# Kernel tuning notes

Hardware: AMD Instinct MI355X
Metric: run time of the kernel (lower is better)

The kernel has to match this reference:

```python
import jax, jax.numpy as jnp
import numpy as np

H = 1024  # hidden_size
V = 32000  # vocab_size
L = 2048  # y_len


def _lstm_cell(gates, c):
    # torch gate order: input, forget, cell(g), output
    i = jax.nn.sigmoid(gates[:H])
    f = jax.nn.sigmoid(gates[H:2 * H])
    g = jnp.tanh(gates[2 * H:3 * H])
    o = jax.nn.sigmoid(gates[3 * H:4 * H])
    c_new = f * c + i * g
    return o * jnp.tanh(c_new), c_new


def setup_inputs() -> dict:
    key = jax.random.key(0)
    ks = jax.random.split(key, 13)
    s = 0.05
    inp = {
        "y": jax.random.randint(ks[0], (L,), 0, V, dtype=jnp.int32),
        "context_vector": jax.random.normal(ks[1], (2, H), dtype=jnp.float32),
        # layer 0: input dim 1
        "w_ih0": jax.random.normal(ks[2], (4 * H, 1), dtype=jnp.float32) * s,
        "w_hh0": jax.random.normal(ks[3], (4 * H, H), dtype=jnp.float32) * s,
        "b_ih0": jax.random.normal(ks[4], (4 * H,), dtype=jnp.float32) * s,
        "b_hh0": jax.random.normal(ks[5], (4 * H,), dtype=jnp.float32) * s,
        # layer 1: input dim H
        "w_ih1": jax.random.normal(ks[6], (4 * H, H), dtype=jnp.float32) * s,
        "w_hh1": jax.random.normal(ks[7], (4 * H, H), dtype=jnp.float32) * s,
        "b_ih1": jax.random.normal(ks[8], (4 * H,), dtype=jnp.float32) * s,
        "b_hh1": jax.random.normal(ks[9], (4 * H,), dtype=jnp.float32) * s,
        # fc: hidden -> vocab
        "w_fc": jax.random.normal(ks[10], (V, H), dtype=jnp.float32) * s,
        "b_fc": jax.random.normal(ks[11], (V,), dtype=jnp.float32) * s,
    }
    return inp


def reference(y, context_vector, w_ih0, w_hh0, b_ih0, b_hh0,
              w_ih1, w_hh1, b_ih1, b_hh1, w_fc, b_fc):
    # tfr = 0.0 => teacher forcing never used; next input is argmax of predictions.
    # h_s = h_c = context_vector initially (as in the torch module).
    def step(carry, _):
        tok, h, c = carry  # tok: scalar f32; h,c: [2, H]
        x = tok[None]  # [1]
        g0 = w_ih0 @ x + b_ih0 + w_hh0 @ h[0] + b_hh0
        h0, c0 = _lstm_cell(g0, c[0])
        g1 = w_ih1 @ h0 + b_ih1 + w_hh1 @ h[1] + b_hh1
        h1, c1 = _lstm_cell(g1, c[1])
        preds = jax.nn.relu(w_fc @ h1 + b_fc)  # [V]
        best = jnp.argmax(preds).astype(jnp.float32)
        return (best, jnp.stack([h0, h1]), jnp.stack([c0, c1])), preds

    init = (y[0].astype(jnp.float32), context_vector, context_vector)
    _, preds_seq = jax.lax.scan(step, init, None, length=L - 1)  # [L-1, V]
    outputs = jnp.concatenate(
        [jnp.zeros((1, V), dtype=jnp.float32), preds_seq], axis=0)  # [L, V]
    return outputs  # training mode: raw outputs (eval would apply log_softmax)
```

## Files before the change

kernel.cpp:

```cpp
#include <hip/hip_runtime.h>
#include <cstdint>
#include <cstddef>

#define H   1024
#define V   32000
#define L   2048
#define G4  4096
#define NB  256
#define NT  1024
#define RPB (V / NB)

#define GNB   500
#define GT    512
#define GS    8
#define GR    8
#define NCHUNK (L / GS)

__device__ __forceinline__ float wave_reduce_sum(float v) {
    #pragma unroll
    for (int off = 32; off > 0; off >>= 1) v += __shfl_down(v, off);
    return v;
}

__device__ __forceinline__ float wave_reduce_max(float v) {
    #pragma unroll
    for (int off = 32; off > 0; off >>= 1) v = fmaxf(v, __shfl_down(v, off));
    return v;
}

__device__ __forceinline__ unsigned long long wave_reduce_max_u64(unsigned long long v) {
    #pragma unroll
    for (int off = 32; off > 0; off >>= 1) {
        const unsigned long long o = __shfl_down(v, off);
        v = (o > v) ? o : v;
    }
    return v;
}

__device__ __forceinline__ float sigmoidf_(float x) {
    return 1.0f / (1.0f + expf(-x));
}

__device__ __forceinline__ float dot4(const float4 w, const float* __restrict__ h, int c) {
    return w.x * h[c] + w.y * h[c + 1] + w.z * h[c + 2] + w.w * h[c + 3];
}

__device__ __forceinline__ float sb2f(int w, int pos) {
    return (float)((w << ((3 - pos) * 8)) >> 24);
}

__global__ __launch_bounds__(256) void quant_fc(
    const float* __restrict__ src, signed char* __restrict__ dst,
    float2* __restrict__ scl_eps, unsigned int* __restrict__ emax_bits)
{
    const int gw   = (blockIdx.x * blockDim.x + threadIdx.x) >> 6;
    const int lane = threadIdx.x & 63;
    const int nw   = (gridDim.x * blockDim.x) >> 6;
    for (int row = gw; row < V; row += nw) {
        const float* p = src + (size_t)row * H + lane * 16;
        float w[16];
        #pragma unroll
        for (int j = 0; j < 4; j++) {
            const float4 f = *(const float4*)(p + j * 4);
            w[j * 4 + 0] = f.x; w[j * 4 + 1] = f.y;
            w[j * 4 + 2] = f.z; w[j * 4 + 3] = f.w;
        }
        float m = 0.f;
        #pragma unroll
        for (int j = 0; j < 16; j++) m = fmaxf(m, fabsf(w[j]));
        m = wave_reduce_max(m);
        m = __shfl(m, 0);
        const float scale = fmaxf(m, 1e-30f) / 127.f;
        const float inv   = 127.f / fmaxf(m, 1e-30f);
        int q[16];
        float esq = 0.f;
        #pragma unroll
        for (int j = 0; j < 16; j++) {
            q[j] = __float2int_rn(w[j] * inv);
            const float e = w[j] - scale * (float)q[j];
            esq += e * e;
        }
        esq = wave_reduce_sum(esq);
        const unsigned int d0 = (q[0] & 255) | ((q[1] & 255) << 8) | ((q[2] & 255) << 16) | ((unsigned int)(q[3] & 255) << 24);
        const unsigned int d1 = (q[4] & 255) | ((q[5] & 255) << 8) | ((q[6] & 255) << 16) | ((unsigned int)(q[7] & 255) << 24);
        const unsigned int d2 = (q[8] & 255) | ((q[9] & 255) << 8) | ((q[10] & 255) << 16) | ((unsigned int)(q[11] & 255) << 24);
        const unsigned int d3 = (q[12] & 255) | ((q[13] & 255) << 8) | ((q[14] & 255) << 16) | ((unsigned int)(q[15] & 255) << 24);
        *(int4*)(dst + (size_t)row * H + lane * 16) =
            make_int4((int)d0, (int)d1, (int)d2, (int)d3);
        if (lane == 0) {
            const float e2 = sqrtf(esq) + 1e-12f;
            scl_eps[row] = make_float2(scale, e2);
            atomicMax(emax_bits, __float_as_uint(e2));
        }
    }
}

__global__ __launch_bounds__(NT) void init_kernel(
    const int* __restrict__ y, const float* __restrict__ ctx,
    const float* __restrict__ w_hh0, const float* __restrict__ b_ih0,
    const float* __restrict__ b_hh0,
    const float* __restrict__ w_hh1, const float* __restrict__ b_ih1,
    const float* __restrict__ b_hh1,
    float* __restrict__ v0, float* __restrict__ u1,
    float* __restrict__ c0, float* __restrict__ c1,
    float* __restrict__ h1g, unsigned long long* __restrict__ keys)
{
    __shared__ __align__(16) float h0s[H];
    __shared__ __align__(16) float h1s[H];
    const int b = blockIdx.x, t = threadIdx.x;
    h0s[t] = ctx[t];
    h1s[t] = ctx[H + t];
    __syncthreads();

    const int wave = t >> 6, lane = t & 63;
    const int rowR = (wave >> 2) * H + b * 4 + (wave & 3);
    {
        const float* w0r = w_hh0 + (size_t)rowR * H;
        const float* w1r = w_hh1 + (size_t)rowR * H;
        float accV = 0.f, accU = 0.f;
        #pragma unroll
        for (int k = 0; k < 4; k++) {
            const int c = k * 256 + lane * 4;
            accV += dot4(*(const float4*)(w0r + c), h0s, c);
            accU += dot4(*(const float4*)(w1r + c), h1s, c);
        }
        accV = wave_reduce_sum(accV);
        accU = wave_reduce_sum(accU);
        if (lane == 0) {
            v0[rowR] = accV + b_ih0[rowR] + b_hh0[rowR];
            u1[rowR] = accU + b_ih1[rowR] + b_hh1[rowR];
        }
    }
    if (b == 0) {
        c0[t]  = ctx[t];
        c1[t]  = ctx[H + t];
        h1g[t] = ctx[H + t];
        if (t < NB) keys[t] = 0ull;
        if (t == 0) {
            keys[0] = ((unsigned long long)0x7F800000u << 32) |
                      (0xFFFFFFFFu - (unsigned int)y[0]);
        }
    }
}

__global__ __launch_bounds__(NT) void lstm_kernel(
    const float* __restrict__ w_ih0, const float* __restrict__ w_ih1,
    const float* __restrict__ w_hh0,
    const float* __restrict__ b_ih0, const float* __restrict__ b_hh0,
    const float* __restrict__ v0_in, float* __restrict__ v0_out,
    const float* __restrict__ u1,
    const float* __restrict__ c0_in, float* __restrict__ c0_out,
    float* __restrict__ c1, float* __restrict__ h1g,
    const unsigned long long* __restrict__ keys,
    float* __restrict__ h1_hist, const int step)
{
    __shared__ __align__(16) float h0s[H];
    __shared__ float g1s[16];
    __shared__ unsigned long long kred[4];
    const int b = blockIdx.x, t = threadIdx.x;
    const int wave = t >> 6, lane = t & 63;

    if (wave < 4) {
        unsigned long long k = keys[t];
        k = wave_reduce_max_u64(k);
        if (lane == 0) kred[wave] = k;
    }
    __syncthreads();
    unsigned long long kk = kred[0];
    kk = (kred[1] > kk) ? kred[1] : kk;
    kk = (kred[2] > kk) ? kred[2] : kk;
    kk = (kred[3] > kk) ? kred[3] : kk;
    const float tok =
        (float)(unsigned int)(0xFFFFFFFFu - (unsigned int)(kk & 0xFFFFFFFFull));

    {
        const float gi = v0_in[t]         + tok * w_ih0[t];
        const float gf = v0_in[H + t]     + tok * w_ih0[H + t];
        const float gg = v0_in[2 * H + t] + tok * w_ih0[2 * H + t];
        const float go = v0_in[3 * H + t] + tok * w_ih0[3 * H + t];
        const float i_ = sigmoidf_(gi);
        const float f_ = sigmoidf_(gf);
        const float g_ = tanhf(gg);
        const float o_ = sigmoidf_(go);
        const float cn = f_ * c0_in[t] + i_ * g_;
        if (b == 0) c0_out[t] = cn;
        h0s[t] = o_ * tanhf(cn);
    }
    __syncthreads();

    const int rowR = (wave >> 2) * H + b * 4 + (wave & 3);
    {
        const float* wA = w_ih1 + (size_t)rowR * H;
        const float* wB = w_hh0 + (size_t)rowR * H;
        float accA = 0.f, accB = 0.f;
        #pragma unroll
        for (int k = 0; k < 4; k++) {
            const int c = k * 256 + lane * 4;
            accA += dot4(*(const float4*)(wA + c), h0s, c);
            accB += dot4(*(const float4*)(wB + c), h0s, c);
        }
        accA = wave_reduce_sum(accA);
        accB = wave_reduce_sum(accB);
        if (lane == 0) {
            g1s[wave]    = accA + u1[rowR];
            v0_out[rowR] = accB + b_ih0[rowR] + b_hh0[rowR];
        }
    }
    __syncthreads();

    if (t < 4) {
        const float i_ = sigmoidf_(g1s[t]);
        const float f_ = sigmoidf_(g1s[4 + t]);
        const float g_ = tanhf(g1s[8 + t]);
        const float o_ = sigmoidf_(g1s[12 + t]);
        const float cn = f_ * c1[b * 4 + t] + i_ * g_;
        c1[b * 4 + t] = cn;
        const float hv = o_ * tanhf(cn);
        h1g[b * 4 + t] = hv;
        if (h1_hist) h1_hist[(size_t)step * H + b * 4 + t] = hv;
    }
}

__global__ __launch_bounds__(NT) void screen_kernel(
    const signed char* __restrict__ wq8, const float2* __restrict__ scl_eps,
    const unsigned int* __restrict__ emax_bits,
    const float* __restrict__ w_fc, const float* __restrict__ b_fc,
    const float* __restrict__ w_hh1, const float* __restrict__ b_ih1,
    const float* __restrict__ b_hh1,
    const float* __restrict__ h1g, float* __restrict__ u1,
    unsigned long long* __restrict__ keys)
{
    __shared__ __align__(16) float h1s[H];
    __shared__ float aprx[128];
    __shared__ float red[16];
    __shared__ float Amax_s, Hl2_s;
    __shared__ unsigned long long wkey[16];
    const int b = blockIdx.x, t = threadIdx.x;
    const int wave = t >> 6, lane = t & 63;

    h1s[t] = h1g[t];
    if (t < 128) aprx[t] = -1.f;
    __syncthreads();

    {
        float sq = h1s[t] * h1s[t];
        sq = wave_reduce_sum(sq);
        if (lane == 0) red[wave] = sq;
    }

    const float4 hA = *(const float4*)(h1s + lane * 16);
    const float4 hB = *(const float4*)(h1s + lane * 16 + 4);
    const float4 hC = *(const float4*)(h1s + lane * 16 + 8);
    const float4 hD = *(const float4*)(h1s + lane * 16 + 12);

    #pragma unroll
    for (int i = 0; i < 8; i++) {
        const int rl = i * 16 + wave;
        if (rl >= RPB) break;
        const int row = b * RPB + rl;
        const int4 qv = *(const int4*)(wq8 + (size_t)row * H + lane * 16);
        float acc;
        acc  = sb2f(qv.x, 0) * hA.x + sb2f(qv.x, 1) * hA.y + sb2f(qv.x, 2) * hA.z + sb2f(qv.x, 3) * hA.w;
        acc += sb2f(qv.y, 0) * hB.x + sb2f(qv.y, 1) * hB.y + sb2f(qv.y, 2) * hB.z + sb2f(qv.y, 3) * hB.w;
        acc += sb2f(qv.z, 0) * hC.x + sb2f(qv.z, 1) * hC.y + sb2f(qv.z, 2) * hC.z + sb2f(qv.z, 3) * hC.w;
        acc += sb2f(qv.w, 0) * hD.x + sb2f(qv.w, 1) * hD.y + sb2f(qv.w, 2) * hD.z + sb2f(qv.w, 3) * hD.w;
        acc = wave_reduce_sum(acc);
        if (lane == 0) {
            float p = scl_eps[row].x * acc + b_fc[row];
            p = p > 0.f ? p : 0.f;
            aprx[rl] = p;
        }
    }
    __syncthreads();

    if (t == 0) {
        float s = 0.f;
        #pragma unroll
        for (int i = 0; i < 16; i++) s += red[i];
        Hl2_s = sqrtf(s);
    }
    if (wave == 0) {
        float m = fmaxf(aprx[lane], aprx[lane + 64]);
        m = wave_reduce_max(m);
        if (lane == 0) Amax_s = m;
    }
    __syncthreads();

    const float emax   = __uint_as_float(*emax_bits);
    const float thresh = Amax_s - (2.f * emax * Hl2_s + 1e-3f);

    unsigned long long bestKey = 0ull;

    #pragma unroll
    for (int i = 0; i < 8; i++) {
        const int rl = i * 16 + wave;
        if (rl >= RPB) break;
        const float av = aprx[rl];
        if (av >= thresh) {
            const int row = b * RPB + rl;
            const float* wrow = w_fc + (size_t)row * H;
            float acc = 0.f;
            #pragma unroll
            for (int k = 0; k < 4; k++) {
                const int c = k * 256 + lane * 4;
                acc += dot4(*(const float4*)(wrow + c), h1s, c);
            }
            acc = wave_reduce_sum(acc);
            if (lane == 0) {
                float p = acc + b_fc[row];
                p = p > 0.f ? p : 0.f;
                const unsigned long long key =
                    ((unsigned long long)__float_as_uint(p) << 32) |
                    (0xFFFFFFFFu - (unsigned int)row);
                if (key > bestKey) bestKey = key;
            }
        }
    }

    {
        const int rowR = (wave >> 2) * H + b * 4 + (wave & 3);
        const float* wrow = w_hh1 + (size_t)rowR * H;
        float acc = 0.f;
        #pragma unroll
        for (int k = 0; k < 4; k++) {
            const int c = k * 256 + lane * 4;
            acc += dot4(*(const float4*)(wrow + c), h1s, c);
        }
        acc = wave_reduce_sum(acc);
        if (lane == 0) u1[rowR] = acc + b_ih1[rowR] + b_hh1[rowR];
    }

    if (lane == 0) wkey[wave] = bestKey;
    __syncthreads();
    if (t == 0) {
        unsigned long long k = wkey[0];
        #pragma unroll
        for (int i = 1; i < 16; i++) k = (wkey[i] > k) ? wkey[i] : k;
        keys[b] = k;
    }
}

__global__ __launch_bounds__(NT) void fc32_kernel(
    const float* __restrict__ w_fc, const float* __restrict__ b_fc,
    const float* __restrict__ w_hh1, const float* __restrict__ b_ih1,
    const float* __restrict__ b_hh1,
    const float* __restrict__ h1g, float* __restrict__ u1,
    unsigned long long* __restrict__ keys, float* __restrict__ out_row)
{
    __shared__ __align__(16) float h1s[H];
    __shared__ unsigned long long wkey[16];
    const int b = blockIdx.x, t = threadIdx.x;
    const int wave = t >> 6, lane = t & 63;

    h1s[t] = h1g[t];
    __syncthreads();

    unsigned long long bestKey = 0ull;
    #pragma unroll
    for (int i = 0; i < 8; i++) {
        const int rl = i * 16 + wave;
        if (rl >= RPB) break;
        const int row = b * RPB + rl;
        const float* wrow = w_fc + (size_t)row * H;
        float acc = 0.f;
        #pragma unroll
        for (int k = 0; k < 4; k++) {
            const int c = k * 256 + lane * 4;
            acc += dot4(*(const float4*)(wrow + c), h1s, c);
        }
        acc = wave_reduce_sum(acc);
        if (lane == 0) {
            float p = acc + b_fc[row];
            p = p > 0.f ? p : 0.f;
            out_row[row] = p;
            const unsigned long long key =
                ((unsigned long long)__float_as_uint(p) << 32) |
                (0xFFFFFFFFu - (unsigned int)row);
            if (key > bestKey) bestKey = key;
        }
    }

    {
        const int rowR = (wave >> 2) * H + b * 4 + (wave & 3);
        const float* wrow = w_hh1 + (size_t)rowR * H;
        float acc = 0.f;
        #pragma unroll
        for (int k = 0; k < 4; k++) {
            const int c = k * 256 + lane * 4;
            acc += dot4(*(const float4*)(wrow + c), h1s, c);
        }
        acc = wave_reduce_sum(acc);
        if (lane == 0) u1[rowR] = acc + b_ih1[rowR] + b_hh1[rowR];
    }

    if (lane == 0) wkey[wave] = bestKey;
    __syncthreads();
    if (t == 0) {
        unsigned long long k = wkey[0];
        #pragma unroll
        for (int i = 1; i < 16; i++) k = (wkey[i] > k) ? wkey[i] : k;
        keys[b] = k;
    }
}

__global__ __launch_bounds__(GT) void out_gemm(
    const float* __restrict__ w_fc, const float* __restrict__ b_fc,
    const float* __restrict__ h1_hist, float* __restrict__ out)
{
    __shared__ __align__(16) float hs[GS][H];
    __shared__ float stage[GS][64];
    const int b = blockIdx.x, t = threadIdx.x;
    const int wave = t >> 6, lane = t & 63;
    const int row0 = b * 64 + wave * GR;

    float4 wr[GR][4];
    #pragma unroll
    for (int r = 0; r < GR; r++)
        #pragma unroll
        for (int k = 0; k < 4; k++)
            wr[r][k] = *(const float4*)(w_fc + (size_t)(row0 + r) * H + k * 256 + lane * 4);

    for (int chunk = 0; chunk < NCHUNK; ++chunk) {
        __syncthreads();
        {
            const float4* src = (const float4*)(h1_hist + (size_t)chunk * GS * H);
            float4* dsts = (float4*)(&hs[0][0]);
            #pragma unroll
            for (int j = 0; j < 4; j++) dsts[j * GT + t] = src[j * GT + t];
        }
        __syncthreads();

        #pragma unroll
        for (int sb = 0; sb < 2; sb++) {
            float acc[GR][4];
            #pragma unroll
            for (int r = 0; r < GR; r++)
                #pragma unroll
                for (int s = 0; s < 4; s++) acc[r][s] = 0.f;
            #pragma unroll
            for (int k = 0; k < 4; k++) {
                const int c = k * 256 + lane * 4;
                const float4 h0 = *(const float4*)(&hs[sb * 4 + 0][c]);
                const float4 h1 = *(const float4*)(&hs[sb * 4 + 1][c]);
                const float4 h2 = *(const float4*)(&hs[sb * 4 + 2][c]);
                const float4 h3 = *(const float4*)(&hs[sb * 4 + 3][c]);
                #pragma unroll
                for (int r = 0; r < GR; r++) {
                    const float4 w = wr[r][k];
                    acc[r][0] += w.x * h0.x + w.y * h0.y + w.z * h0.z + w.w * h0.w;
                    acc[r][1] += w.x * h1.x + w.y * h1.y + w.z * h1.z + w.w * h1.w;
                    acc[r][2] += w.x * h2.x + w.y * h2.y + w.z * h2.z + w.w * h2.w;
                    acc[r][3] += w.x * h3.x + w.y * h3.y + w.z * h3.z + w.w * h3.w;
                }
            }
            #pragma unroll
            for (int r = 0; r < GR; r++)
                #pragma unroll
                for (int s = 0; s < 4; s++) {
                    const float vv = wave_reduce_sum(acc[r][s]);
                    if (lane == 0) stage[sb * 4 + s][wave * GR + r] = vv;
                }
        }
        __syncthreads();
        {
            const int s = t >> 6;
            const int col = t & 63;
            const int sidx = chunk * GS + s;
            if (sidx >= 1) {
                const float vv = stage[s][col] + b_fc[b * 64 + col];
                out[(size_t)sidx * V + b * 64 + col] = fmaxf(vv, 0.f);
            }
        }
    }
}

extern "C" void kernel_launch(void* const* d_in, const int* in_sizes, int n_in,
                              void* d_out, int out_size, void* d_ws, size_t ws_size,
                              hipStream_t stream)
{
    const int*   y     = (const int*)  d_in[0];
    const float* ctx   = (const float*)d_in[1];
    const float* w_ih0 = (const float*)d_in[2];
    const float* w_hh0 = (const float*)d_in[3];
    const float* b_ih0 = (const float*)d_in[4];
    const float* b_hh0 = (const float*)d_in[5];
    const float* w_ih1 = (const float*)d_in[6];
    const float* w_hh1 = (const float*)d_in[7];
    const float* b_ih1 = (const float*)d_in[8];
    const float* b_hh1 = (const float*)d_in[9];
    const float* w_fc  = (const float*)d_in[10];
    const float* b_fc  = (const float*)d_in[11];
    float* out = (float*)d_out;

    const size_t WQ8_BYTES  = (size_t)V * H;
    const size_t SCL_BYTES  = (size_t)V * sizeof(float2);
    const size_t HIST_BYTES = (size_t)L * H * sizeof(float);
    const size_t STATE_BYTES = 67600;
    const int use8 = (ws_size >= WQ8_BYTES + SCL_BYTES + HIST_BYTES + STATE_BYTES) ? 1 : 0;

    char* ws = (char*)d_ws;
    signed char* wq8     = (signed char*)ws;
    float2*      scl_eps = (float2*)(ws + WQ8_BYTES);
    float*       h1_hist = (float*)(ws + WQ8_BYTES + SCL_BYTES);
    char* base = ws + (use8 ? (WQ8_BYTES + SCL_BYTES + HIST_BYTES) : 0);
    float* v0g = (float*)(base + 0);
    float* u1  = (float*)(base + 32768);
    float* c0  = (float*)(base + 49152);
    float* c1  = (float*)(base + 57344);
    float* h1g = (float*)(base + 61440);
    unsigned long long* keys = (unsigned long long*)(base + 65536);
    unsigned int* emax_bits  = (unsigned int*)(base + 67584);

    hipMemsetAsync(d_out, 0, (size_t)V * sizeof(float), stream);

    if (use8) {
        hipMemsetAsync(emax_bits, 0, 8, stream);
        hipMemsetAsync(h1_hist, 0, (size_t)H * sizeof(float), stream);
        quant_fc<<<512, 256, 0, stream>>>(w_fc, wq8, scl_eps, emax_bits);
    }

    init_kernel<<<NB, NT, 0, stream>>>(y, ctx, w_hh0, b_ih0, b_hh0,
                                       w_hh1, b_ih1, b_hh1,
                                       v0g, u1, c0, c1, h1g, keys);

    for (int t = 1; t < L; t++) {
        const float* v0i = v0g + ((t - 1) & 1) * G4;
        float*       v0o = v0g + (t & 1) * G4;
        const float* c0i = c0 + ((t - 1) & 1) * H;
        float*       c0o = c0 + (t & 1) * H;
        lstm_kernel<<<NB, NT, 0, stream>>>(w_ih0, w_ih1, w_hh0, b_ih0, b_hh0,
                                           v0i, v0o, u1, c0i, c0o, c1, h1g, keys,
                                           use8 ? h1_hist : (float*)nullptr, t);
        if (use8) {
            screen_kernel<<<NB, NT, 0, stream>>>(wq8, scl_eps, emax_bits,
                                                 w_fc, b_fc,
                                                 w_hh1, b_ih1, b_hh1,
                                                 h1g, u1, keys);
        } else {
            fc32_kernel<<<NB, NT, 0, stream>>>(w_fc, b_fc,
                                               w_hh1, b_ih1, b_hh1,
                                               h1g, u1, keys,
                                               out + (size_t)t * V);
        }
    }

    if (use8) {
        out_gemm<<<GNB, GT, 0, stream>>>(w_fc, b_fc, h1_hist, out);
    }
}
```

Before: 60.11 ms.

## Move w_hh1 matvec into LSTM kernel and tighten per-row screening bounds

Moves the layer-1 recurrent matvec (w_hh1·h1) from the screen/fc kernels into the LSTM kernel, prefetching its weights before the first barrier and double-buffering h1. The screen kernel now uses per-row error bounds (upper bound against the block-wide maximum lower bound) in place of a global max-error threshold, so fewer rows should need exact fp32 recomputation. It also batches the int8 row loads and shuffle reductions across eight rows for more memory-level parallelism. In exchange the LSTM kernel does more work and holds more registers, and the screen kernel drops an atomic and a global error scalar.

```diff
diff --git a/kernel.cpp b/kernel.cpp
--- a/kernel.cpp
+++ b/kernel.cpp
@@ -51,7 +51,7 @@
 
 __global__ __launch_bounds__(256) void quant_fc(
     const float* __restrict__ src, signed char* __restrict__ dst,
-    float2* __restrict__ scl_eps, unsigned int* __restrict__ emax_bits)
+    float2* __restrict__ scl_eps)
 {
     const int gw   = (blockIdx.x * blockDim.x + threadIdx.x) >> 6;
     const int lane = threadIdx.x & 63;
@@ -88,9 +88,7 @@
         *(int4*)(dst + (size_t)row * H + lane * 16) =
             make_int4((int)d0, (int)d1, (int)d2, (int)d3);
         if (lane == 0) {
-            const float e2 = sqrtf(esq) + 1e-12f;
-            scl_eps[row] = make_float2(scale, e2);
-            atomicMax(emax_bits, __float_as_uint(e2));
+            scl_eps[row] = make_float2(scale, sqrtf(esq) + 1e-12f);
         }
     }
 }
@@ -99,42 +97,31 @@
     const int* __restrict__ y, const float* __restrict__ ctx,
     const float* __restrict__ w_hh0, const float* __restrict__ b_ih0,
     const float* __restrict__ b_hh0,
-    const float* __restrict__ w_hh1, const float* __restrict__ b_ih1,
-    const float* __restrict__ b_hh1,
-    float* __restrict__ v0, float* __restrict__ u1,
-    float* __restrict__ c0, float* __restrict__ c1,
-    float* __restrict__ h1g, unsigned long long* __restrict__ keys)
+    float* __restrict__ v0, float* __restrict__ c0, float* __restrict__ c1,
+    float* __restrict__ h1g0, unsigned long long* __restrict__ keys)
 {
     __shared__ __align__(16) float h0s[H];
-    __shared__ __align__(16) float h1s[H];
     const int b = blockIdx.x, t = threadIdx.x;
     h0s[t] = ctx[t];
-    h1s[t] = ctx[H + t];
     __syncthreads();
 
     const int wave = t >> 6, lane = t & 63;
     const int rowR = (wave >> 2) * H + b * 4 + (wave & 3);
     {
         const float* w0r = w_hh0 + (size_t)rowR * H;
-        const float* w1r = w_hh1 + (size_t)rowR * H;
-        float accV = 0.f, accU = 0.f;
+        float accV = 0.f;
         #pragma unroll
         for (int k = 0; k < 4; k++) {
             const int c = k * 256 + lane * 4;
             accV += dot4(*(const float4*)(w0r + c), h0s, c);
-            accU += dot4(*(const float4*)(w1r + c), h1s, c);
         }
         accV = wave_reduce_sum(accV);
-        accU = wave_reduce_sum(accU);
-        if (lane == 0) {
-            v0[rowR] = accV + b_ih0[rowR] + b_hh0[rowR];
-            u1[rowR] = accU + b_ih1[rowR] + b_hh1[rowR];
-        }
+        if (lane == 0) v0[rowR] = accV + b_ih0[rowR] + b_hh0[rowR];
     }
     if (b == 0) {
-        c0[t]  = ctx[t];
-        c1[t]  = ctx[H + t];
-        h1g[t] = ctx[H + t];
+        c0[t]   = ctx[t];
+        c1[t]   = ctx[H + t];
+        h1g0[t] = ctx[H + t];
         if (t < NB) keys[t] = 0ull;
         if (t == 0) {
             keys[0] = ((unsigned long long)0x7F800000u << 32) |
@@ -145,27 +132,46 @@
 
 __global__ __launch_bounds__(NT) void lstm_kernel(
     const float* __restrict__ w_ih0, const float* __restrict__ w_ih1,
-    const float* __restrict__ w_hh0,
+    const float* __restrict__ w_hh0, const float* __restrict__ w_hh1,
     const float* __restrict__ b_ih0, const float* __restrict__ b_hh0,
+    const float* __restrict__ b_ih1, const float* __restrict__ b_hh1,
     const float* __restrict__ v0_in, float* __restrict__ v0_out,
-    const float* __restrict__ u1,
     const float* __restrict__ c0_in, float* __restrict__ c0_out,
-    float* __restrict__ c1, float* __restrict__ h1g,
+    float* __restrict__ c1,
+    const float* __restrict__ h1prev, float* __restrict__ h1out,
     const unsigned long long* __restrict__ keys,
     float* __restrict__ h1_hist, const int step)
 {
     __shared__ __align__(16) float h0s[H];
+    __shared__ __align__(16) float h1ps[H];
     __shared__ float g1s[16];
     __shared__ unsigned long long kred[4];
     const int b = blockIdx.x, t = threadIdx.x;
     const int wave = t >> 6, lane = t & 63;
+    const int rowR = (wave >> 2) * H + b * 4 + (wave & 3);
+
+    const float* wU = w_hh1 + (size_t)rowR * H;
+    float4 wu[4];
+    #pragma unroll
+    for (int k = 0; k < 4; k++)
+        wu[k] = *(const float4*)(wU + k * 256 + lane * 4);
+
+    h1ps[t] = h1prev[t];
 
     if (wave < 4) {
         unsigned long long k = keys[t];
         k = wave_reduce_max_u64(k);
         if (lane == 0) kred[wave] = k;
     }
-    __syncthreads();
+
+    const float v0a = v0_in[t],         v0b = v0_in[H + t];
+    const float v0c = v0_in[2 * H + t], v0d = v0_in[3 * H + t];
+    const float wia = w_ih0[t],         wib = w_ih0[H + t];
+    const float wic = w_ih0[2 * H + t], wid = w_ih0[3 * H + t];
+    const float c0v = c0_in[t];
+
+    __syncthreads();
+
     unsigned long long kk = kred[0];
     kk = (kred[1] > kk) ? kred[1] : kk;
     kk = (kred[2] > kk) ? kred[2] : kk;
@@ -173,22 +179,28 @@
     const float tok =
         (float)(unsigned int)(0xFFFFFFFFu - (unsigned int)(kk & 0xFFFFFFFFull));
 
+    float accU = 0.f;
+    #pragma unroll
+    for (int k = 0; k < 4; k++) {
+        const int c = k * 256 + lane * 4;
+        accU += dot4(wu[k], h1ps, c);
+    }
+
     {
-        const float gi = v0_in[t]         + tok * w_ih0[t];
-        const float gf = v0_in[H + t]     + tok * w_ih0[H + t];
-        const float gg = v0_in[2 * H + t] + tok * w_ih0[2 * H + t];
-        const float go = v0_in[3 * H + t] + tok * w_ih0[3 * H + t];
+        const float gi = v0a + tok * wia;
+        const float gf = v0b + tok * wib;
+        const float gg = v0c + tok * wic;
+        const float go = v0d + tok * wid;
         const float i_ = sigmoidf_(gi);
         const float f_ = sigmoidf_(gf);
         const float g_ = tanhf(gg);
         const float o_ = sigmoidf_(go);
-        const float cn = f_ * c0_in[t] + i_ * g_;
+        const float cn = f_ * c0v + i_ * g_;
         if (b == 0) c0_out[t] = cn;
         h0s[t] = o_ * tanhf(cn);
     }
     __syncthreads();
 
-    const int rowR = (wave >> 2) * H + b * 4 + (wave & 3);
     {
         const float* wA = w_ih1 + (size_t)rowR * H;
         const float* wB = w_hh0 + (size_t)rowR * H;
@@ -199,11 +211,11 @@
             accA += dot4(*(const float4*)(wA + c), h0s, c);
             accB += dot4(*(const float4*)(wB + c), h0s, c);
         }
-        accA = wave_reduce_sum(accA);
-        accB = wave_reduce_sum(accB);
+        const float g  = wave_reduce_sum(accA + accU);
+        const float vv = wave_reduce_sum(accB);
         if (lane == 0) {
-            g1s[wave]    = accA + u1[rowR];
-            v0_out[rowR] = accB + b_ih0[rowR] + b_hh0[rowR];
+            g1s[wave]    = g  + b_ih1[rowR] + b_hh1[rowR];
+            v0_out[rowR] = vv + b_ih0[rowR] + b_hh0[rowR];
         }
     }
     __syncthreads();
@@ -216,36 +228,39 @@
         const float cn = f_ * c1[b * 4 + t] + i_ * g_;
         c1[b * 4 + t] = cn;
         const float hv = o_ * tanhf(cn);
-        h1g[b * 4 + t] = hv;
+        h1out[b * 4 + t] = hv;
         if (h1_hist) h1_hist[(size_t)step * H + b * 4 + t] = hv;
     }
 }
 
 __global__ __launch_bounds__(NT) void screen_kernel(
     const signed char* __restrict__ wq8, const float2* __restrict__ scl_eps,
-    const unsigned int* __restrict__ emax_bits,
     const float* __restrict__ w_fc, const float* __restrict__ b_fc,
-    const float* __restrict__ w_hh1, const float* __restrict__ b_ih1,
-    const float* __restrict__ b_hh1,
-    const float* __restrict__ h1g, float* __restrict__ u1,
-    unsigned long long* __restrict__ keys)
+    const float* __restrict__ h1cur, unsigned long long* __restrict__ keys)
 {
     __shared__ __align__(16) float h1s[H];
-    __shared__ float aprx[128];
+    __shared__ float lb[128], ub[128];
     __shared__ float red[16];
-    __shared__ float Amax_s, Hl2_s;
+    __shared__ float LBmax_s;
     __shared__ unsigned long long wkey[16];
     const int b = blockIdx.x, t = threadIdx.x;
     const int wave = t >> 6, lane = t & 63;
 
-    h1s[t] = h1g[t];
-    if (t < 128) aprx[t] = -1.f;
-    __syncthreads();
-
+    const float hv = h1cur[t];
+    h1s[t] = hv;
+    if (t < 128) { lb[t] = -3e38f; ub[t] = -3e38f; }
     {
-        float sq = h1s[t] * h1s[t];
-        sq = wave_reduce_sum(sq);
+        const float sq = wave_reduce_sum(hv * hv);
         if (lane == 0) red[wave] = sq;
+    }
+    __syncthreads();
+
+    float Hl2;
+    {
+        float s = 0.f;
+        #pragma unroll
+        for (int i = 0; i < 16; i++) s += red[i];
+        Hl2 = sqrtf(s);
     }
 
     const float4 hA = *(const float4*)(h1s + lane * 16);
@@ -253,61 +268,72 @@
     const float4 hC = *(const float4*)(h1s + lane * 16 + 8);
     const float4 hD = *(const float4*)(h1s + lane * 16 + 12);
 
+    int4 qv[8];
+    #pragma unroll
+    for (int i = 0; i < 8; i++) {
+        const int rl = i * 16 + wave;
+        const int row = b * RPB + (rl < RPB ? rl : 0);
+        qv[i] = *(const int4*)(wq8 + (size_t)row * H + lane * 16);
+    }
+    float acc[8];
+    #pragma unroll
+    for (int i = 0; i < 8; i++) {
+        const int4 q = qv[i];
+        float a;
+        a  = sb2f(q.x, 0) * hA.x + sb2f(q.x, 1) * hA.y + sb2f(q.x, 2) * hA.z + sb2f(q.x, 3) * hA.w;
+        a += sb2f(q.y, 0) * hB.x + sb2f(q.y, 1) * hB.y + sb2f(q.y, 2) * hB.z + sb2f(q.y, 3) * hB.w;
+        a += sb2f(q.z, 0) * hC.x + sb2f(q.z, 1) * hC.y + sb2f(q.z, 2) * hC.z + sb2f(q.z, 3) * hC.w;
+        a += sb2f(q.w, 0) * hD.x + sb2f(q.w, 1) * hD.y + sb2f(q.w, 2) * hD.z + sb2f(q.w, 3) * hD.w;
+        acc[i] = a;
+    }
+    #pragma unroll
+    for (int off = 32; off > 0; off >>= 1) {
+        #pragma unroll
+        for (int i = 0; i < 8; i++) acc[i] += __shfl_down(acc[i], off);
+    }
+    if (lane == 0) {
+        #pragma unroll
+        for (int i = 0; i < 8; i++) {
+            const int rl = i * 16 + wave;
+            if (rl < RPB) {
+                const int row = b * RPB + rl;
+                const float2 se = scl_eps[row];
+                float p = se.x * acc[i] + b_fc[row];
+                p = fmaxf(p, 0.f);
+                const float e = se.y * Hl2;
+                ub[rl] = p + e;
+                lb[rl] = p - e;
+            }
+        }
+    }
+    __syncthreads();
+
+    if (wave == 0) {
+        float m = fmaxf(lb[lane], lb[lane + 64]);
+        m = wave_reduce_max(m);
+        if (lane == 0) LBmax_s = m;
+    }
+    __syncthreads();
+    const float LBmax = LBmax_s;
+
+    unsigned long long bestKey = 0ull;
+
     #pragma unroll
     for (int i = 0; i < 8; i++) {
         const int rl = i * 16 + wave;
         if (rl >= RPB) break;
-        const int row = b * RPB + rl;
-        const int4 qv = *(const int4*)(wq8 + (size_t)row * H + lane * 16);
-        float acc;
-        acc  = sb2f(qv.x, 0) * hA.x + sb2f(qv.x, 1) * hA.y + sb2f(qv.x, 2) * hA.z + sb2f(qv.x, 3) * hA.w;
-        acc += sb2f(qv.y, 0) * hB.x + sb2f(qv.y, 1) * hB.y + sb2f(qv.y, 2) * hB.z + sb2f(qv.y, 3) * hB.w;
-        acc += sb2f(qv.z, 0) * hC.x + sb2f(qv.z, 1) * hC.y + sb2f(qv.z, 2) * hC.z + sb2f(qv.z, 3) * hC.w;
-        acc += sb2f(qv.w, 0) * hD.x + sb2f(qv.w, 1) * hD.y + sb2f(qv.w, 2) * hD.z + sb2f(qv.w, 3) * hD.w;
-        acc = wave_reduce_sum(acc);
-        if (lane == 0) {
-            float p = scl_eps[row].x * acc + b_fc[row];
-            p = p > 0.f ? p : 0.f;
-            aprx[rl] = p;
-        }
-    }
-    __syncthreads();
-
-    if (t == 0) {
-        float s = 0.f;
-        #pragma unroll
-        for (int i = 0; i < 16; i++) s += red[i];
-        Hl2_s = sqrtf(s);
-    }
-    if (wave == 0) {
-        float m = fmaxf(aprx[lane], aprx[lane + 64]);
-        m = wave_reduce_max(m);
-        if (lane == 0) Amax_s = m;
-    }
-    __syncthreads();
-
-    const float emax   = __uint_as_float(*emax_bits);
-    const float thresh = Amax_s - (2.f * emax * Hl2_s + 1e-3f);
-
-    unsigned long long bestKey = 0ull;
-
-    #pragma unroll
-    for (int i = 0; i < 8; i++) {
-        const int rl = i * 16 + wave;
-        if (rl >= RPB) break;
-        const float av = aprx[rl];
-        if (av >= thresh) {
+        if (ub[rl] >= LBmax) {
             const int row = b * RPB + rl;
             const float* wrow = w_fc + (size_t)row * H;
-            float acc = 0.f;
+            float a = 0.f;
             #pragma unroll
             for (int k = 0; k < 4; k++) {
                 const int c = k * 256 + lane * 4;
-                acc += dot4(*(const float4*)(wrow + c), h1s, c);
+                a += dot4(*(const float4*)(wrow + c), h1s, c);
             }
-            acc = wave_reduce_sum(acc);
+            a = wave_reduce_sum(a);
             if (lane == 0) {
-                float p = acc + b_fc[row];
+                float p = a + b_fc[row];
                 p = p > 0.f ? p : 0.f;
                 const unsigned long long key =
                     ((unsigned long long)__float_as_uint(p) << 32) |
@@ -317,19 +343,6 @@
         }
     }
 
-    {
-        const int rowR = (wave >> 2) * H + b * 4 + (wave & 3);
-        const float* wrow = w_hh1 + (size_t)rowR * H;
-        float acc = 0.f;
-        #pragma unroll
-        for (int k = 0; k < 4; k++) {
-            const int c = k * 256 + lane * 4;
-            acc += dot4(*(const float4*)(wrow + c), h1s, c);
-        }
-        acc = wave_reduce_sum(acc);
-        if (lane == 0) u1[rowR] = acc + b_ih1[rowR] + b_hh1[rowR];
-    }
-
     if (lane == 0) wkey[wave] = bestKey;
     __syncthreads();
     if (t == 0) {
@@ -342,17 +355,15 @@
 
 __global__ __launch_bounds__(NT) void fc32_kernel(
     const float* __restrict__ w_fc, const float* __restrict__ b_fc,
-    const float* __restrict__ w_hh1, const float* __restrict__ b_ih1,
-    const float* __restrict__ b_hh1,
-    const float* __restrict__ h1g, float* __restrict__ u1,
-    unsigned long long* __restrict__ keys, float* __restrict__ out_row)
+    const float* __restrict__ h1cur, unsigned long long* __restrict__ keys,
+    float* __restrict__ out_row)
 {
     __shared__ __align__(16) float h1s[H];
     __shared__ unsigned long long wkey[16];
     const int b = blockIdx.x, t = threadIdx.x;
     const int wave = t >> 6, lane = t & 63;
 
-    h1s[t] = h1g[t];
+    h1s[t] = h1cur[t];
     __syncthreads();
 
     unsigned long long bestKey = 0ull;
@@ -362,15 +373,15 @@
         if (rl >= RPB) break;
         const int row = b * RPB + rl;
         const float* wrow = w_fc + (size_t)row * H;
-        float acc = 0.f;
+        float a = 0.f;
         #pragma unroll
         for (int k = 0; k < 4; k++) {
             const int c = k * 256 + lane * 4;
-            acc += dot4(*(const float4*)(wrow + c), h1s, c);
-        }
-        acc = wave_reduce_sum(acc);
+            a += dot4(*(const float4*)(wrow + c), h1s, c);
+        }
+        a = wave_reduce_sum(a);
         if (lane == 0) {
-            float p = acc + b_fc[row];
+            float p = a + b_fc[row];
             p = p > 0.f ? p : 0.f;
             out_row[row] = p;
             const unsigned long long key =
@@ -378,19 +389,6 @@
                 (0xFFFFFFFFu - (unsigned int)row);
             if (key > bestKey) bestKey = key;
         }
-    }
-
-    {
-        const int rowR = (wave >> 2) * H + b * 4 + (wave & 3);
-        const float* wrow = w_hh1 + (size_t)rowR * H;
-        float acc = 0.f;
-        #pragma unroll
-        for (int k = 0; k < 4; k++) {
-            const int c = k * 256 + lane * 4;
-            acc += dot4(*(const float4*)(wrow + c), h1s, c);
-        }
-        acc = wave_reduce_sum(acc);
-        if (lane == 0) u1[rowR] = acc + b_ih1[rowR] + b_hh1[rowR];
     }
 
     if (lane == 0) wkey[wave] = bestKey;
@@ -495,7 +493,7 @@
     const size_t WQ8_BYTES  = (size_t)V * H;
     const size_t SCL_BYTES  = (size_t)V * sizeof(float2);
     const size_t HIST_BYTES = (size_t)L * H * sizeof(float);
-    const size_t STATE_BYTES = 67600;
+    const size_t STATE_BYTES = 55296;
     const int use8 = (ws_size >= WQ8_BYTES + SCL_BYTES + HIST_BYTES + STATE_BYTES) ? 1 : 0;
 
     char* ws = (char*)d_ws;
@@ -504,42 +502,38 @@
     float*       h1_hist = (float*)(ws + WQ8_BYTES + SCL_BYTES);
     char* base = ws + (use8 ? (WQ8_BYTES + SCL_BYTES + HIST_BYTES) : 0);
     float* v0g = (float*)(base + 0);
-    float* u1  = (float*)(base + 32768);
-    float* c0  = (float*)(base + 49152);
-    float* c1  = (float*)(base + 57344);
-    float* h1g = (float*)(base + 61440);
-    unsigned long long* keys = (unsigned long long*)(base + 65536);
-    unsigned int* emax_bits  = (unsigned int*)(base + 67584);
+    float* c0  = (float*)(base + 32768);
+    float* c1  = (float*)(base + 40960);
+    float* h1g = (float*)(base + 45056);
+    unsigned long long* keys = (unsigned long long*)(base + 53248);
 
     hipMemsetAsync(d_out, 0, (size_t)V * sizeof(float), stream);
 
     if (use8) {
-        hipMemsetAsync(emax_bits, 0, 8, stream);
         hipMemsetAsync(h1_hist, 0, (size_t)H * sizeof(float), stream);
-        quant_fc<<<512, 256, 0, stream>>>(w_fc, wq8, scl_eps, emax_bits);
+        quant_fc<<<512, 256, 0, stream>>>(w_fc, wq8, scl_eps);
     }
 
     init_kernel<<<NB, NT, 0, stream>>>(y, ctx, w_hh0, b_ih0, b_hh0,
-                                       w_hh1, b_ih1, b_hh1,
-                                       v0g, u1, c0, c1, h1g, keys);
+                                       v0g, c0, c1, h1g , keys);
 
     for (int t = 1; t < L; t++) {
         const float* v0i = v0g + ((t - 1) & 1) * G4;
         float*       v0o = v0g + (t & 1) * G4;
         const float* c0i = c0 + ((t - 1) & 1) * H;
         float*       c0o = c0 + (t & 1) * H;
-        lstm_kernel<<<NB, NT, 0, stream>>>(w_ih0, w_ih1, w_hh0, b_ih0, b_hh0,
-                                           v0i, v0o, u1, c0i, c0o, c1, h1g, keys,
+        const float* h1p = h1g + ((t - 1) & 1) * H;
+        float*       h1c = h1g + (t & 1) * H;
+        lstm_kernel<<<NB, NT, 0, stream>>>(w_ih0, w_ih1, w_hh0, w_hh1,
+                                           b_ih0, b_hh0, b_ih1, b_hh1,
+                                           v0i, v0o, c0i, c0o, c1,
+                                           h1p, h1c, keys,
                                            use8 ? h1_hist : (float*)nullptr, t);
         if (use8) {
-            screen_kernel<<<NB, NT, 0, stream>>>(wq8, scl_eps, emax_bits,
-                                                 w_fc, b_fc,
-                                                 w_hh1, b_ih1, b_hh1,
-                                                 h1g, u1, keys);
+            screen_kernel<<<NB, NT, 0, stream>>>(wq8, scl_eps, w_fc, b_fc,
+                                                 h1c, keys);
         } else {
-            fc32_kernel<<<NB, NT, 0, stream>>>(w_fc, b_fc,
-                                               w_hh1, b_ih1, b_hh1,
-                                               h1g, u1, keys,
+            fc32_kernel<<<NB, NT, 0, stream>>>(w_fc, b_fc, h1c, keys,
                                                out + (size_t)t * V);
         }
     }
```

New measurement: 53.54 ms. -10.9%, faster.
